# Kernel optimization log

Measured on AMD Instinct MI355X. Metric: run time of the kernel, lower is better.

Reference implementation:

```python
import jax, jax.numpy as jnp
import numpy as np

B, IN, OUT = 8192, 1024, 1024


def setup_inputs() -> dict:
    key = jax.random.key(0)
    k1, k2 = jax.random.split(key)
    x = jax.random.normal(k1, (B, IN), dtype=jnp.float32)
    W_seed = jax.random.normal(k2, (IN, OUT), dtype=jnp.float32) / np.sqrt(IN).astype(np.float32)
    b_seed = jnp.zeros((OUT,), dtype=jnp.float32)
    W_sig = jnp.zeros((2,), dtype=jnp.float32)  # mixture logits over ['dense','Toeplitz']
    b_sig = jnp.zeros((2,), dtype=jnp.float32)  # mixture logits over ['dense','None']
    A_sig = jnp.zeros((2,), dtype=jnp.float32)  # mixture logits over ['linear','relu']
    return {"x": x, "W_seed": W_seed, "b_seed": b_seed,
            "W_sig": W_sig, "b_sig": b_sig, "A_sig": A_sig}


def _toeplitz_from_seed(W_seed):
    # seed_vec = [W_seed[0, out-1], ..., W_seed[0, 1], W_seed[0,0], ..., W_seed[in-1,0]]
    in_sz, out_sz = W_seed.shape
    seed_vec = jnp.concatenate([W_seed[0, -1:0:-1], W_seed[:, 0]])  # [out-1 + in]
    # W_toep[i, j] = seed_vec[i - j + out - 1]
    idx = jnp.arange(in_sz)[:, None] - jnp.arange(out_sz)[None, :] + (out_sz - 1)
    return seed_vec[idx]  # [in, out]


def reference(x, W_seed, b_seed, W_sig, b_sig, A_sig):
    W_toep = _toeplitz_from_seed(W_seed)
    w_s = jax.nn.softmax(W_sig)
    W_core = w_s[0] * W_seed + w_s[1] * W_toep          # softmax-weighted weight mixture
    b_s = jax.nn.softmax(b_sig)
    b_core = b_s[0] * b_seed                             # 'None' branch contributes zeros
    out = x @ W_core + b_core                            # [B, out]
    a_s = jax.nn.softmax(A_sig)
    return a_s[0] * out + a_s[1] * jax.nn.relu(out)      # activation mixture
```

## Files before the change

### kernel.cpp

```cpp
#include <hip/hip_runtime.h>

typedef unsigned short ushort_t;
typedef __bf16 bf16x8 __attribute__((ext_vector_type(8)));
typedef float f32x4 __attribute__((ext_vector_type(4)));

#define AS1 __attribute__((address_space(1)))
#define AS3 __attribute__((address_space(3)))

__device__ __forceinline__ ushort_t f2bf(float f) {
    unsigned u = __builtin_bit_cast(unsigned, f);
    u = (u + 0x7fffu + ((u >> 16) & 1u)) >> 16;
    return (ushort_t)u;
}

__device__ __forceinline__ void async16(void* lds, const void* g) {
    __builtin_amdgcn_global_load_lds((const AS1 unsigned int*)g,
                                     (AS3 unsigned int*)lds, 16, 0, 0);
}

__device__ __forceinline__ void softmax2(const float* __restrict__ sig, float& s0, float& s1) {
    float a = sig[0], b = sig[1];
    float m = fmaxf(a, b);
    float e0 = __expf(a - m), e1 = __expf(b - m);
    float inv = 1.0f / (e0 + e1);
    s0 = e0 * inv; s1 = e1 * inv;
}

__device__ __forceinline__ float toep_val(const float* __restrict__ Wseed, int k, int o) {
    return (k >= o) ? Wseed[(size_t)(k - o) << 10] : Wseed[o - k];
}

__global__ __launch_bounds__(256) void prep_kernel(const float* __restrict__ x,
                                                   const float* __restrict__ Wseed,
                                                   const float* __restrict__ Wsig,
                                                   ushort_t* __restrict__ xb,
                                                   ushort_t* __restrict__ Wt) {
    int b = blockIdx.x;
    if (b < 4096) {
        int i = b * 256 + threadIdx.x;
        const float4* xp = (const float4*)x + (size_t)i * 2;
        float4 a = xp[0], c = xp[1];
        uint4 r;
        r.x = (unsigned)f2bf(a.x) | ((unsigned)f2bf(a.y) << 16);
        r.y = (unsigned)f2bf(a.z) | ((unsigned)f2bf(a.w) << 16);
        r.z = (unsigned)f2bf(c.x) | ((unsigned)f2bf(c.y) << 16);
        r.w = (unsigned)f2bf(c.z) | ((unsigned)f2bf(c.w) << 16);
        ((uint4*)xb)[i] = r;
        return;
    }
    __shared__ float T[64][65];
    int bb = b - 4096;
    int k0 = (bb >> 4) * 64;
    int o0 = (bb & 15) * 64;
    int t = threadIdx.x;
    #pragma unroll
    for (int i = 0; i < 4; ++i) {
        int lin = t + i * 256;
        int kr = lin >> 4;
        int c4 = lin & 15;
        float4 v = *(const float4*)&Wseed[(size_t)(k0 + kr) * 1024 + o0 + c4 * 4];
        T[kr][c4 * 4 + 0] = v.x;
        T[kr][c4 * 4 + 1] = v.y;
        T[kr][c4 * 4 + 2] = v.z;
        T[kr][c4 * 4 + 3] = v.w;
    }
    __syncthreads();
    float s0, s1; softmax2(Wsig, s0, s1);
    #pragma unroll
    for (int i = 0; i < 2; ++i) {
        int lin = t + i * 256;
        int oo = lin >> 3;
        int kq = (lin & 7) * 8;
        unsigned r[4];
        #pragma unroll
        for (int q = 0; q < 4; ++q) {
            float v0 = s0 * T[kq + 2 * q + 0][oo] + s1 * toep_val(Wseed, k0 + kq + 2 * q + 0, o0 + oo);
            float v1 = s0 * T[kq + 2 * q + 1][oo] + s1 * toep_val(Wseed, k0 + kq + 2 * q + 1, o0 + oo);
            r[q] = (unsigned)f2bf(v0) | ((unsigned)f2bf(v1) << 16);
        }
        *(uint4*)&Wt[(size_t)(o0 + oo) * 1024 + k0 + kq] = make_uint4(r[0], r[1], r[2], r[3]);
    }
}

#define BM 128
#define BN 128
#define BK 32
#define NKT 32

__global__ __launch_bounds__(256, 2) void gemm_kernel(const ushort_t* __restrict__ Xb,
                                                      const ushort_t* __restrict__ Wt,
                                                      const float* __restrict__ bseed,
                                                      const float* __restrict__ bsig,
                                                      const float* __restrict__ asig,
                                                      float* __restrict__ out) {
    __shared__ ushort_t lds[16384];
    ushort_t* At0 = lds;
    ushort_t* Bt0 = lds + 4096;
    ushort_t* At1 = lds + 8192;
    ushort_t* Bt1 = lds + 12288;

    const int t = threadIdx.x;
    const int wv = t >> 6;
    const int lane = t & 63;

    const int orig = blockIdx.x;
    const int g = orig & 7;
    const int within = orig >> 3;
    const int rb = g * 8 + (within >> 3);
    const int cb = within & 7;
    const int brow = rb * BM;
    const int bcol = cb * BN;

    const int r0 = t >> 2;
    const int kc = (t & 3) * 8;
    const ushort_t* gA0 = Xb + (size_t)(brow + r0) * 1024 + kc;
    const ushort_t* gA1 = Xb + (size_t)(brow + 64 + r0) * 1024 + kc;
    const ushort_t* gB0 = Wt + (size_t)(bcol + r0) * 1024 + kc;
    const ushort_t* gB1 = Wt + (size_t)(bcol + 64 + r0) * 1024 + kc;

    f32x4 acc[4][4];
    #pragma unroll
    for (int i = 0; i < 4; ++i)
        #pragma unroll
        for (int j = 0; j < 4; ++j) acc[i][j] = (f32x4){0.f, 0.f, 0.f, 0.f};

    const int wr = (wv >> 1) * 64;
    const int wcn = (wv & 1) * 64;
    const int fr = lane & 15;
    const int kg = (lane >> 4) * 8;

    float bs0, bs1, as0, as1;
    softmax2(bsig, bs0, bs1);
    softmax2(asig, as0, as1);
    float bias[4];
    #pragma unroll
    for (int ni = 0; ni < 4; ++ni)
        bias[ni] = bs0 * bseed[bcol + wcn + ni * 16 + fr];
    asm volatile("" :: "v"(bias[0]), "v"(bias[1]), "v"(bias[2]), "v"(bias[3]),
                       "v"(as0), "v"(as1));
    asm volatile("" ::: "memory");

    const int sA = wv * 512;
    const int sA2 = 2048 + wv * 512;
#define STAGE(Abuf, Bbuf, ko)                                  \
    do {                                                       \
        async16((Abuf) + sA,  gA0 + (ko));                     \
        async16((Abuf) + sA2, gA1 + (ko));                     \
        async16((Bbuf) + sA,  gB0 + (ko));                     \
        async16((Bbuf) + sA2, gB1 + (ko));                     \
    } while (0)

#define COMPUTE(Abuf, Bbuf)                                                        \
    do {                                                                           \
        bf16x8 af[4], bf[4];                                                       \
        _Pragma("unroll")                                                          \
        for (int mi = 0; mi < 4; ++mi)                                             \
            af[mi] = *(const bf16x8*)&(Abuf)[(wr + mi * 16 + fr) * BK + kg];       \
        _Pragma("unroll")                                                          \
        for (int ni = 0; ni < 4; ++ni)                                             \
            bf[ni] = *(const bf16x8*)&(Bbuf)[(wcn + ni * 16 + fr) * BK + kg];      \
        _Pragma("unroll")                                                          \
        for (int mi = 0; mi < 4; ++mi)                                             \
            _Pragma("unroll")                                                      \
            for (int ni = 0; ni < 4; ++ni)                                         \
                acc[mi][ni] = __builtin_amdgcn_mfma_f32_16x16x32_bf16(             \
                    af[mi], bf[ni], acc[mi][ni], 0, 0, 0);                         \
    } while (0)

#define WAIT4() asm volatile("s_waitcnt vmcnt(4)" ::: "memory")
#define WAIT0() asm volatile("s_waitcnt vmcnt(0)" ::: "memory")
#define BAR()   __builtin_amdgcn_s_barrier()
#define PIN()   __builtin_amdgcn_sched_barrier(0)

    STAGE(At0, Bt0, 0);
    for (int it = 0; it < 15; ++it) {
        STAGE(At1, Bt1, (2 * it + 1) * BK);
        WAIT4(); BAR(); PIN();
        COMPUTE(At0, Bt0);
        BAR();
        STAGE(At0, Bt0, (2 * it + 2) * BK);
        WAIT4(); BAR(); PIN();
        COMPUTE(At1, Bt1);
        BAR();
    }
    STAGE(At1, Bt1, 31 * BK);
    WAIT4(); BAR(); PIN();
    COMPUTE(At0, Bt0);
    WAIT0(); BAR(); PIN();
    COMPUTE(At1, Bt1);

    #pragma unroll
    for (int ni = 0; ni < 4; ++ni) {
        int col = bcol + wcn + ni * 16 + fr;
        #pragma unroll
        for (int mi = 0; mi < 4; ++mi) {
            int row = brow + wr + mi * 16 + (lane >> 4) * 4;
            #pragma unroll
            for (int r = 0; r < 4; ++r) {
                float v = acc[mi][ni][r] + bias[ni];
                out[(size_t)(row + r) * 1024 + col] = as0 * v + as1 * fmaxf(v, 0.f);
            }
        }
    }
#undef STAGE
#undef COMPUTE
#undef WAIT4
#undef WAIT0
#undef BAR
#undef PIN
}

__global__ __launch_bounds__(256) void naive_kernel(const float* __restrict__ x,
                                                    const float* __restrict__ Wseed,
                                                    const float* __restrict__ bseed,
                                                    const float* __restrict__ Wsig,
                                                    const float* __restrict__ bsig,
                                                    const float* __restrict__ asig,
                                                    float* __restrict__ out) {
    int idx = blockIdx.x * 256 + threadIdx.x;
    int b = idx >> 10, o = idx & 1023;
    float ws0, ws1, bs0, bs1, as0, as1;
    softmax2(Wsig, ws0, ws1);
    softmax2(bsig, bs0, bs1);
    softmax2(asig, as0, as1);
    float s = 0.f;
    const float* xr = x + (size_t)b * 1024;
    for (int k = 0; k < 1024; ++k) {
        float wc = ws0 * Wseed[((size_t)k << 10) + o] + ws1 * toep_val(Wseed, k, o);
        s += xr[k] * wc;
    }
    float v = s + bs0 * bseed[o];
    out[idx] = as0 * v + as1 * fmaxf(v, 0.f);
}

extern "C" void kernel_launch(void* const* d_in, const int* in_sizes, int n_in,
                              void* d_out, int out_size, void* d_ws, size_t ws_size,
                              hipStream_t stream) {
    const float* x     = (const float*)d_in[0];
    const float* Wseed = (const float*)d_in[1];
    const float* bseed = (const float*)d_in[2];
    const float* Wsig  = (const float*)d_in[3];
    const float* bsig  = (const float*)d_in[4];
    const float* Asig  = (const float*)d_in[5];
    float* out = (float*)d_out;

    const size_t need = (2u << 20) + (16u << 20) + 1024;
    if (ws_size < need) {
        naive_kernel<<<dim3(8192 * 1024 / 256), dim3(256), 0, stream>>>(
            x, Wseed, bseed, Wsig, bsig, Asig, out);
        return;
    }

    ushort_t* Wt = (ushort_t*)d_ws;
    ushort_t* Xb = (ushort_t*)((char*)d_ws + (2u << 20));

    prep_kernel<<<dim3(4096 + 256), dim3(256), 0, stream>>>(x, Wseed, Wsig, Xb, Wt);
    gemm_kernel<<<dim3(512), dim3(256), 0, stream>>>(Xb, Wt, bseed, bsig, Asig, out);
}
```

Baseline: 43.11 us.

## Double K-tile to 64 with XOR-swizzled LDS and simpler double-buffer sync

Raises the GEMM K tile from 32 to 64, which halves the number of pipeline iterations and doubles LDS to 64KB per block. The async global-to-LDS loads now place each 16-byte chunk at a slot XOR-swizzled by row, and the fragment reads undo the swizzle, so ds_read accesses should avoid bank conflicts. The split waits and sched barriers are replaced by one full vmcnt/lgkmcnt wait plus a barrier after each compute. This aims to cut barrier and loop overhead per unit of MFMA work, but the full wait may expose more load latency, and the larger LDS footprint could limit occupancy.

```diff
diff --git a/kernel.cpp b/kernel.cpp
--- a/kernel.cpp
+++ b/kernel.cpp
@@ -84,8 +84,8 @@
 
 #define BM 128
 #define BN 128
-#define BK 32
-#define NKT 32
+#define BK 64
+#define NKT 16
 
 __global__ __launch_bounds__(256, 2) void gemm_kernel(const ushort_t* __restrict__ Xb,
                                                       const ushort_t* __restrict__ Wt,
@@ -93,11 +93,11 @@
                                                       const float* __restrict__ bsig,
                                                       const float* __restrict__ asig,
                                                       float* __restrict__ out) {
-    __shared__ ushort_t lds[16384];
+    __shared__ ushort_t lds[32768];
     ushort_t* At0 = lds;
-    ushort_t* Bt0 = lds + 4096;
-    ushort_t* At1 = lds + 8192;
-    ushort_t* Bt1 = lds + 12288;
+    ushort_t* Bt0 = lds + 8192;
+    ushort_t* At1 = lds + 16384;
+    ushort_t* Bt1 = lds + 24576;
 
     const int t = threadIdx.x;
     const int wv = t >> 6;
@@ -111,12 +111,10 @@
     const int brow = rb * BM;
     const int bcol = cb * BN;
 
-    const int r0 = t >> 2;
-    const int kc = (t & 3) * 8;
-    const ushort_t* gA0 = Xb + (size_t)(brow + r0) * 1024 + kc;
-    const ushort_t* gA1 = Xb + (size_t)(brow + 64 + r0) * 1024 + kc;
-    const ushort_t* gB0 = Wt + (size_t)(bcol + r0) * 1024 + kc;
-    const ushort_t* gB1 = Wt + (size_t)(bcol + 64 + r0) * 1024 + kc;
+    const int rs = t >> 3;
+    const int cs = (t & 7) ^ (rs & 7);
+    const ushort_t* gA = Xb + (size_t)(brow + rs) * 1024 + 8 * cs;
+    const ushort_t* gB = Wt + (size_t)(bcol + rs) * 1024 + 8 * cs;
 
     f32x4 acc[4][4];
     #pragma unroll
@@ -127,7 +125,7 @@
     const int wr = (wv >> 1) * 64;
     const int wcn = (wv & 1) * 64;
     const int fr = lane & 15;
-    const int kg = (lane >> 4) * 8;
+    const int kq = lane >> 4;
 
     float bs0, bs1, as0, as1;
     softmax2(bsig, bs0, bs1);
@@ -140,53 +138,58 @@
                        "v"(as0), "v"(as1));
     asm volatile("" ::: "memory");
 
-    const int sA = wv * 512;
-    const int sA2 = 2048 + wv * 512;
-#define STAGE(Abuf, Bbuf, ko)                                  \
-    do {                                                       \
-        async16((Abuf) + sA,  gA0 + (ko));                     \
-        async16((Abuf) + sA2, gA1 + (ko));                     \
-        async16((Bbuf) + sA,  gB0 + (ko));                     \
-        async16((Bbuf) + sA2, gB1 + (ko));                     \
+#define STAGE1(buf, gptr, ko)                                      \
+    do {                                                           \
+        async16((buf) + wv * 512,        (gptr) + (ko));           \
+        async16((buf) + 2048 + wv * 512, (gptr) + 32768 + (ko));   \
+        async16((buf) + 4096 + wv * 512, (gptr) + 65536 + (ko));   \
+        async16((buf) + 6144 + wv * 512, (gptr) + 98304 + (ko));   \
     } while (0)
+
+#define STAGE(Abuf, Bbuf, ko) do { STAGE1(Abuf, gA, ko); STAGE1(Bbuf, gB, ko); } while (0)
 
 #define COMPUTE(Abuf, Bbuf)                                                        \
     do {                                                                           \
-        bf16x8 af[4], bf[4];                                                       \
+        bf16x8 af[4][2], bf[4][2];                                                 \
         _Pragma("unroll")                                                          \
-        for (int mi = 0; mi < 4; ++mi)                                             \
-            af[mi] = *(const bf16x8*)&(Abuf)[(wr + mi * 16 + fr) * BK + kg];       \
+        for (int mi = 0; mi < 4; ++mi) {                                           \
+            int row_ = wr + mi * 16 + fr;                                          \
+            af[mi][0] = *(const bf16x8*)&(Abuf)[row_ * 64 + (((kq)     ^ (row_ & 7)) << 3)]; \
+            af[mi][1] = *(const bf16x8*)&(Abuf)[row_ * 64 + (((kq + 4) ^ (row_ & 7)) << 3)]; \
+        }                                                                          \
         _Pragma("unroll")                                                          \
-        for (int ni = 0; ni < 4; ++ni)                                             \
-            bf[ni] = *(const bf16x8*)&(Bbuf)[(wcn + ni * 16 + fr) * BK + kg];      \
+        for (int ni = 0; ni < 4; ++ni) {                                           \
+            int row_ = wcn + ni * 16 + fr;                                         \
+            bf[ni][0] = *(const bf16x8*)&(Bbuf)[row_ * 64 + (((kq)     ^ (row_ & 7)) << 3)]; \
+            bf[ni][1] = *(const bf16x8*)&(Bbuf)[row_ * 64 + (((kq + 4) ^ (row_ & 7)) << 3)]; \
+        }                                                                          \
         _Pragma("unroll")                                                          \
         for (int mi = 0; mi < 4; ++mi)                                             \
             _Pragma("unroll")                                                      \
-            for (int ni = 0; ni < 4; ++ni)                                         \
+            for (int ni = 0; ni < 4; ++ni) {                                       \
                 acc[mi][ni] = __builtin_amdgcn_mfma_f32_16x16x32_bf16(             \
-                    af[mi], bf[ni], acc[mi][ni], 0, 0, 0);                         \
+                    af[mi][0], bf[ni][0], acc[mi][ni], 0, 0, 0);                   \
+                acc[mi][ni] = __builtin_amdgcn_mfma_f32_16x16x32_bf16(             \
+                    af[mi][1], bf[ni][1], acc[mi][ni], 0, 0, 0);                   \
+            }                                                                      \
     } while (0)
 
-#define WAIT4() asm volatile("s_waitcnt vmcnt(4)" ::: "memory")
-#define WAIT0() asm volatile("s_waitcnt vmcnt(0)" ::: "memory")
-#define BAR()   __builtin_amdgcn_s_barrier()
-#define PIN()   __builtin_amdgcn_sched_barrier(0)
+#define SYNC() do { asm volatile("s_waitcnt vmcnt(0) lgkmcnt(0)" ::: "memory");    \
+                    __builtin_amdgcn_s_barrier(); } while (0)
 
     STAGE(At0, Bt0, 0);
-    for (int it = 0; it < 15; ++it) {
+    SYNC();
+    for (int it = 0; it < 7; ++it) {
         STAGE(At1, Bt1, (2 * it + 1) * BK);
-        WAIT4(); BAR(); PIN();
         COMPUTE(At0, Bt0);
-        BAR();
+        SYNC();
         STAGE(At0, Bt0, (2 * it + 2) * BK);
-        WAIT4(); BAR(); PIN();
         COMPUTE(At1, Bt1);
-        BAR();
-    }
-    STAGE(At1, Bt1, 31 * BK);
-    WAIT4(); BAR(); PIN();
+        SYNC();
+    }
+    STAGE(At1, Bt1, 15 * BK);
     COMPUTE(At0, Bt0);
-    WAIT0(); BAR(); PIN();
+    SYNC();
     COMPUTE(At1, Bt1);
 
     #pragma unroll
@@ -202,12 +205,10 @@
             }
         }
     }
+#undef STAGE1
 #undef STAGE
 #undef COMPUTE
-#undef WAIT4
-#undef WAIT0
-#undef BAR
-#undef PIN
+#undef SYNC
 }
 
 __global__ __launch_bounds__(256) void naive_kernel(const float* __restrict__ x,
```

Measured after the change: 39.45 us. 1.09x faster.
